# Kernel tuning notes

Measured on AMD Instinct MI355X. Metric: run time of the kernel, lower is better.

## Reference

```python
import jax, jax.numpy as jnp
import numpy as np

TOP_K = 10


def setup_inputs() -> dict:
    key = jax.random.key(0)
    x = jax.random.normal(key, (256, 1, 8192), dtype=jnp.float32)
    return {"x": x}


def reference(x):
    # x: [B, 1, S] real
    B, _, S = x.shape
    # torch.arange(1e-05, 1, 1/S) has exactly S elements for these S
    t = 1e-05 + jnp.arange(S, dtype=jnp.float32) / S            # [S]
    dft = jnp.fft.fft(x[:, 0, :], n=S, axis=-1, norm='ortho')   # [B, S] complex64
    mag = jnp.abs(dft)                                          # [B, S]
    top_idx = jnp.argsort(-mag, axis=-1)[:, :TOP_K]             # [B, k] int
    top_dft = jnp.take_along_axis(dft, top_idx, axis=1)         # [B, k] complex
    # complex exponential basis exp(-2j*pi*k*t), flipped along time
    phase = (-2j * jnp.pi) * (top_idx[:, :, None].astype(jnp.float32) * t[None, None, :])
    bs = jnp.exp(phase)[:, :, ::-1]                             # [B, k, S] complex
    bf = top_dft[:, :, None] * bs / jnp.sqrt(jnp.float32(S))    # [B, k, S]
    # F.pad((1,0), mode='replicate') then crop to S: shift right by 1, duplicate first col
    bf = jnp.concatenate([bf[:, :, :1], bf[:, :, :-1]], axis=-1)
    bf = bf[:, :, None, :]                                      # [B, k, 1, S]
    residual = x - jnp.sum(bf, axis=1)                          # [B, 1, S] complex
    return bf, residual
```

## Files before the change

kernel.cpp:

```cpp
#include <hip/hip_runtime.h>

#define NB    256
#define SLEN  8192
#define LOG2S 13
#define TOPK  10

#define RES_REAL   ((size_t)20971520)
#define FULL_ILV   ((size_t)46137344)

__device__ int   g_k [NB * TOPK];
__device__ float g_ar[NB * TOPK];
__device__ float g_ai[NB * TOPK];

__device__ __forceinline__ float sin_rev(float p) { return __builtin_amdgcn_sinf(p); }
__device__ __forceinline__ float cos_rev(float p) { return __builtin_amdgcn_cosf(p); }

__device__ __forceinline__ bool beats(float om, int oi, float wm, int wi) {
  return (om > wm * 1.0001f) || (om > wm * 0.9999f && oi < wi);
}

__global__ __launch_bounds__(1024)
void fft_topk(const float* __restrict__ x) {
  __shared__ float re[SLEN];
  __shared__ float im[SLEN];
  __shared__ float wred_m[16];
  __shared__ int   wred_i[16];

  const int b = blockIdx.x;
  const int t = threadIdx.x;
  const int lane = t & 63;
  const int wid  = t >> 6;
  const float* xb = x + (size_t)b * SLEN;

  for (int i = t; i < SLEN / 4; i += 1024) {
    const float4 v = ((const float4*)xb)[i];
    *(float4*)&re[i * 4] = v;
    *(float4*)&im[i * 4] = make_float4(0.f, 0.f, 0.f, 0.f);
  }
  __syncthreads();

  for (int i = t; i < SLEN; i += 1024) {
    const int j = (int)(__brev((unsigned)i) >> (32 - LOG2S));
    if (i < j) { const float tmp = re[i]; re[i] = re[j]; re[j] = tmp; }
  }
  __syncthreads();

  for (int stage = 1; stage <= LOG2S; ++stage) {
    const int half = 1 << (stage - 1);
    const float invm = 1.f / (float)(1 << stage);
    for (int bfi = t; bfi < SLEN / 2; bfi += 1024) {
      const int pos = bfi & (half - 1);
      const int i = ((bfi >> (stage - 1)) << stage) + pos;
      const int j = i + half;
      const float p = (float)pos * invm;
      const float c  = cos_rev(p);
      const float sn = -sin_rev(p);
      const float vr = re[j], vi = im[j];
      const float tr = vr * c - vi * sn;
      const float ti = vr * sn + vi * c;
      const float ur = re[i], ui = im[i];
      re[i] = ur + tr; im[i] = ui + ti;
      re[j] = ur - tr; im[j] = ui - ti;
    }
    __syncthreads();
  }

  float m2c[8];
#pragma unroll
  for (int w = 0; w < 8; ++w) {
    const int i = t + (w << 10);
    m2c[w] = re[i] * re[i] + im[i] * im[i];
  }

  for (int sel = 0; sel < TOPK; ++sel) {
    float wm = -1.f; int wi = SLEN;
#pragma unroll
    for (int w = 0; w < 8; ++w) {
      const int i = t + (w << 10);
      if (m2c[w] > wm * 1.0001f) { wm = m2c[w]; wi = i; }
    }
    for (int off = 32; off > 0; off >>= 1) {
      const float om = __shfl_down(wm, off);
      const int   oi = __shfl_down(wi, off);
      if (beats(om, oi, wm, wi)) { wm = om; wi = oi; }
    }
    if (lane == 0) { wred_m[wid] = wm; wred_i[wid] = wi; }
    __syncthreads();
    wm = wred_m[0]; wi = wred_i[0];
    for (int w = 1; w < 16; ++w) {
      const float om = wred_m[w]; const int oi = wred_i[w];
      if (beats(om, oi, wm, wi)) { wm = om; wi = oi; }
    }
    if (t == 0) {
      const float rr = re[wi] * (1.f / (float)SLEN);
      const float ii = im[wi] * (1.f / (float)SLEN);
      const float pr = -1e-5f * (float)wi;
      const float cp = cos_rev(pr), sp = sin_rev(pr);
      g_k [b * TOPK + sel] = wi;
      g_ar[b * TOPK + sel] = rr * cp - ii * sp;
      g_ai[b * TOPK + sel] = rr * sp + ii * cp;
    }
#pragma unroll
    for (int w = 0; w < 8; ++w)
      if (wi == t + (w << 10)) m2c[w] = 0.f;
    __syncthreads();
  }
}

__global__ __launch_bounds__(256, 4)
void gen(const float* __restrict__ x, float* __restrict__ out, size_t cap) {
  const int bs    = blockIdx.x;
  const int b     = bs >> 3;
  const int slice = bs & 7;
  const int t     = threadIdx.x;
  const int s0    = slice * 1024 + t * 4;
  const float* xb = x + (size_t)b * SLEN;

  int kj[TOPK]; float arj[TOPK], aij[TOPK];
#pragma unroll
  for (int j = 0; j < TOPK; ++j) {
    kj[j]  = g_k [b * TOPK + j];
    arj[j] = g_ar[b * TOPK + j];
    aij[j] = g_ai[b * TOPK + j];
  }

  if (cap < FULL_ILV) {
    const size_t bfbase = (size_t)b * TOPK * SLEN;
    const float4 xv = *(const float4*)(xb + s0);
    float acc0 = 0.f, acc1 = 0.f, acc2 = 0.f, acc3 = 0.f;
#pragma unroll
    for (int j = 0; j < TOPK; ++j) {
      const int k = kj[j];
      float br[4];
#pragma unroll
      for (int q = 0; q < 4; ++q) {
        const int s = s0 + q;
        const int m = (s == 0) ? 1 : s;
        const float p = (float)((k * m) & (SLEN - 1)) * (1.f / (float)SLEN);
        br[q] = arj[j] * cos_rev(p) - aij[j] * sin_rev(p);
      }
      acc0 += br[0]; acc1 += br[1]; acc2 += br[2]; acc3 += br[3];
      const size_t o = bfbase + (size_t)j * SLEN + s0;
      if (o + 4 <= cap)
        *(float4*)(out + o) = make_float4(br[0], br[1], br[2], br[3]);
    }
    const size_t o = RES_REAL + (size_t)b * SLEN + s0;
    if (o + 4 <= cap)
      *(float4*)(out + o) =
          make_float4(xv.x - acc0, xv.y - acc1, xv.z - acc2, xv.w - acc3);
  } else {
    const size_t bfbase = (size_t)b * TOPK * SLEN * 2;
    const float4 xv = *(const float4*)(xb + s0);
    float sr[4] = {0.f, 0.f, 0.f, 0.f}, si[4] = {0.f, 0.f, 0.f, 0.f};
#pragma unroll
    for (int j = 0; j < TOPK; ++j) {
      const int k = kj[j];
      float br[4], bi[4];
#pragma unroll
      for (int q = 0; q < 4; ++q) {
        const int s = s0 + q;
        const int m = (s == 0) ? 1 : s;
        const float p = (float)((k * m) & (SLEN - 1)) * (1.f / (float)SLEN);
        const float c = cos_rev(p), sv = sin_rev(p);
        br[q] = arj[j] * c - aij[j] * sv;
        bi[q] = arj[j] * sv + aij[j] * c;
        sr[q] += br[q]; si[q] += bi[q];
      }
      const size_t o = bfbase + ((size_t)j * SLEN + s0) * 2;
      if (o + 8 <= cap) {
        *(float4*)(out + o)     = make_float4(br[0], bi[0], br[1], bi[1]);
        *(float4*)(out + o + 4) = make_float4(br[2], bi[2], br[3], bi[3]);
      }
    }
    const size_t o = (size_t)41943040 + ((size_t)b * SLEN + s0) * 2;
    if (o + 8 <= cap) {
      *(float4*)(out + o)     = make_float4(xv.x - sr[0], -si[0], xv.y - sr[1], -si[1]);
      *(float4*)(out + o + 4) = make_float4(xv.z - sr[2], -si[2], xv.w - sr[3], -si[3]);
    }
  }
}

extern "C" void kernel_launch(void* const* d_in, const int* in_sizes, int n_in,
                              void* d_out, int out_size, void* d_ws, size_t ws_size,
                              hipStream_t stream) {
  const float* x = (const float*)d_in[0];
  float* out = (float*)d_out;
  fft_topk<<<NB, 1024, 0, stream>>>(x);
  gen<<<NB * 8, 256, 0, stream>>>(x, out, (size_t)out_size);
}
```

Measured before the change: 139.4 us.

## Replace radix-2 shared-memory FFT with register radix-8 decimation-in-frequency passes

```diff
diff --git a/kernel.cpp b/kernel.cpp
--- a/kernel.cpp
+++ b/kernel.cpp
@@ -19,10 +19,43 @@
   return (om > wm * 1.0001f) || (om > wm * 0.9999f && oi < wi);
 }
 
+__device__ __forceinline__ int pad(int a) { return a + (a >> 5); }
+
+__device__ __forceinline__ void bfly(float& ur, float& ui, float& vr, float& vi,
+                                     float p) {
+  const float c = cos_rev(p);
+  const float s = -sin_rev(p);
+  const float dr = ur - vr, di = ui - vi;
+  ur += vr; ui += vi;
+  vr = dr * c - di * s;
+  vi = dr * s + di * c;
+}
+
+template<int ST>
+__device__ __forceinline__ void bfly3(float (&xr)[8], float (&xi)[8], int m) {
+  const float inv8 = 1.f / (float)(ST * 8);
+  const float inv4 = 1.f / (float)(ST * 4);
+  const float inv2 = 1.f / (float)(ST * 2);
+#pragma unroll
+  for (int k = 0; k < 4; ++k)
+    bfly(xr[k], xi[k], xr[k + 4], xi[k + 4], (float)(m + ST * k) * inv8);
+#pragma unroll
+  for (int g = 0; g < 2; ++g)
+#pragma unroll
+    for (int k0 = 0; k0 < 2; ++k0) {
+      const int k = g * 4 + k0;
+      bfly(xr[k], xi[k], xr[k + 2], xi[k + 2], (float)(m + ST * k0) * inv4);
+    }
+  const float p1 = (float)m * inv2;
+#pragma unroll
+  for (int k = 0; k < 8; k += 2)
+    bfly(xr[k], xi[k], xr[k + 1], xi[k + 1], p1);
+}
+
 __global__ __launch_bounds__(1024)
 void fft_topk(const float* __restrict__ x) {
-  __shared__ float re[SLEN];
-  __shared__ float im[SLEN];
+  __shared__ float re[8448];
+  __shared__ float im[8448];
   __shared__ float wred_m[16];
   __shared__ int   wred_i[16];
 
@@ -32,52 +65,95 @@
   const int wid  = t >> 6;
   const float* xb = x + (size_t)b * SLEN;
 
-  for (int i = t; i < SLEN / 4; i += 1024) {
-    const float4 v = ((const float4*)xb)[i];
-    *(float4*)&re[i * 4] = v;
-    *(float4*)&im[i * 4] = make_float4(0.f, 0.f, 0.f, 0.f);
-  }
-  __syncthreads();
-
-  for (int i = t; i < SLEN; i += 1024) {
-    const int j = (int)(__brev((unsigned)i) >> (32 - LOG2S));
-    if (i < j) { const float tmp = re[i]; re[i] = re[j]; re[j] = tmp; }
-  }
-  __syncthreads();
-
-  for (int stage = 1; stage <= LOG2S; ++stage) {
-    const int half = 1 << (stage - 1);
-    const float invm = 1.f / (float)(1 << stage);
-    for (int bfi = t; bfi < SLEN / 2; bfi += 1024) {
-      const int pos = bfi & (half - 1);
-      const int i = ((bfi >> (stage - 1)) << stage) + pos;
-      const int j = i + half;
-      const float p = (float)pos * invm;
-      const float c  = cos_rev(p);
-      const float sn = -sin_rev(p);
-      const float vr = re[j], vi = im[j];
-      const float tr = vr * c - vi * sn;
-      const float ti = vr * sn + vi * c;
-      const float ur = re[i], ui = im[i];
-      re[i] = ur + tr; im[i] = ui + ti;
-      re[j] = ur - tr; im[j] = ui - ti;
-    }
-    __syncthreads();
+  float xr[8], xi[8];
+
+#pragma unroll
+  for (int k = 0; k < 8; ++k) { xr[k] = xb[t + (k << 10)]; xi[k] = 0.f; }
+  bfly3<1024>(xr, xi, t);
+#pragma unroll
+  for (int k = 0; k < 8; ++k) {
+    const int a = pad(t + (k << 10));
+    re[a] = xr[k]; im[a] = xi[k];
+  }
+  __syncthreads();
+
+  {
+    const int m  = t & 127;
+    const int i0 = m + ((t >> 7) << 10);
+#pragma unroll
+    for (int k = 0; k < 8; ++k) {
+      const int a = pad(i0 + (k << 7));
+      xr[k] = re[a]; xi[k] = im[a];
+    }
+    bfly3<128>(xr, xi, m);
+#pragma unroll
+    for (int k = 0; k < 8; ++k) {
+      const int a = pad(i0 + (k << 7));
+      re[a] = xr[k]; im[a] = xi[k];
+    }
+  }
+  __syncthreads();
+
+  {
+    const int m  = t & 15;
+    const int i0 = m + ((t >> 4) << 7);
+#pragma unroll
+    for (int k = 0; k < 8; ++k) {
+      const int a = pad(i0 + (k << 4));
+      xr[k] = re[a]; xi[k] = im[a];
+    }
+    bfly3<16>(xr, xi, m);
+#pragma unroll
+    for (int k = 0; k < 8; ++k) {
+      const int a = pad(i0 + (k << 4));
+      re[a] = xr[k]; im[a] = xi[k];
+    }
+  }
+  __syncthreads();
+
+  {
+    const int m  = t & 1;
+    const int i0 = m + ((t >> 1) << 4);
+#pragma unroll
+    for (int k = 0; k < 8; ++k) {
+      const int a = pad(i0 + (k << 1));
+      xr[k] = re[a]; xi[k] = im[a];
+    }
+    bfly3<2>(xr, xi, m);
+#pragma unroll
+    for (int k = 0; k < 8; ++k) {
+      const int a = pad(i0 + (k << 1));
+      re[a] = xr[k]; im[a] = xi[k];
+    }
+  }
+  __syncthreads();
+
+#pragma unroll
+  for (int q = 0; q < 8; ++q) {
+    const int a = pad((t << 3) + q);
+    xr[q] = re[a]; xi[q] = im[a];
+  }
+#pragma unroll
+  for (int q = 0; q < 8; q += 2) {
+    const float ur = xr[q], ui = xi[q];
+    const float vr = xr[q + 1], vi = xi[q + 1];
+    xr[q] = ur + vr;     xi[q] = ui + vi;
+    xr[q + 1] = ur - vr; xi[q + 1] = ui - vi;
   }
 
   float m2c[8];
 #pragma unroll
-  for (int w = 0; w < 8; ++w) {
-    const int i = t + (w << 10);
-    m2c[w] = re[i] * re[i] + im[i] * im[i];
-  }
+  for (int q = 0; q < 8; ++q) m2c[q] = xr[q] * xr[q] + xi[q] * xi[q];
+
+  const int rt = (int)(__brev((unsigned)t) >> 22);
+  const int qord[8] = {0, 4, 2, 6, 1, 5, 3, 7};
 
   for (int sel = 0; sel < TOPK; ++sel) {
     float wm = -1.f; int wi = SLEN;
 #pragma unroll
-    for (int w = 0; w < 8; ++w) {
-      const int i = t + (w << 10);
-      if (m2c[w] > wm * 1.0001f) { wm = m2c[w]; wi = i; }
+    for (int j = 0; j < 8; ++j) {
+      const int q = qord[j];
+      if (m2c[q] > wm * 1.0001f) { wm = m2c[q]; wi = rt + (j << 10); }
     }
     for (int off = 32; off > 0; off >>= 1) {
       const float om = __shfl_down(wm, off);
@@ -91,18 +167,18 @@
       const float om = wred_m[w]; const int oi = wred_i[w];
       if (beats(om, oi, wm, wi)) { wm = om; wi = oi; }
     }
-    if (t == 0) {
-      const float rr = re[wi] * (1.f / (float)SLEN);
-      const float ii = im[wi] * (1.f / (float)SLEN);
+    const int p = (int)(__brev((unsigned)wi) >> 19);
+    if ((p >> 3) == t) {
+      const int q = p & 7;
+      const float rr = xr[q] * (1.f / (float)SLEN);
+      const float ii = xi[q] * (1.f / (float)SLEN);
       const float pr = -1e-5f * (float)wi;
       const float cp = cos_rev(pr), sp = sin_rev(pr);
       g_k [b * TOPK + sel] = wi;
       g_ar[b * TOPK + sel] = rr * cp - ii * sp;
       g_ai[b * TOPK + sel] = rr * sp + ii * cp;
-    }
-#pragma unroll
-    for (int w = 0; w < 8; ++w)
-      if (wi == t + (w << 10)) m2c[w] = 0.f;
+      m2c[q] = 0.f;
+    }
     __syncthreads();
   }
 }
```

Result: faster. 132.1 us (-5.3%).
